# Performance work log

Measured on AMD Instinct MI355X. Metric: run time of the kernel, lower is better.

## Reference

```python
import jax, jax.numpy as jnp
import numpy as np

N = 50000        # nodes
E = 1_600_000    # edges per graph (avg degree 32)
T = 5            # timesteps per node
F_RAW = 395      # 3 meta channels + 392 signal
H_GRU = 64
HID = 40


def setup_inputs() -> dict:
    key = jax.random.key(0)
    ks = jax.random.split(key, 20)
    s = 0.05
    inp = {
        "x": jax.random.normal(ks[0], (N, T, F_RAW), jnp.float32),
        "edge_index": jax.random.randint(ks[1], (2, E), 0, N, dtype=jnp.int32),
        "feat_edge_index": jax.random.randint(ks[2], (2, E), 0, N, dtype=jnp.int32),
        # FeatureCNN: Conv1d(1, 16, kernel_size=40, stride=88) -> L=5 -> flatten 80
        "conv_w": jax.random.normal(ks[3], (16, 1, 40), jnp.float32) * s,
        "conv_b": jnp.zeros((16,), jnp.float32),
        "lin1_w": jax.random.normal(ks[4], (40, 80), jnp.float32) * s,
        "lin1_b": jnp.zeros((40,), jnp.float32),
        # GRU(input=41, hidden=64), PyTorch gate order: r, z, n
        "gru_w_ih": jax.random.normal(ks[5], (3 * H_GRU, 41), jnp.float32) * s,
        "gru_w_hh": jax.random.normal(ks[6], (3 * H_GRU, H_GRU), jnp.float32) * s,
        "gru_b_ih": jnp.zeros((3 * H_GRU,), jnp.float32),
        "gru_b_hh": jnp.zeros((3 * H_GRU,), jnp.float32),
        "gcn1_w": jax.random.normal(ks[7], (104, HID), jnp.float32) * s,
        "gcn1_b": jnp.zeros((HID,), jnp.float32),
        "gcn2_w": jax.random.normal(ks[8], (104, HID), jnp.float32) * s,
        "gcn2_b": jnp.zeros((HID,), jnp.float32),
        "mlp_w": jax.random.normal(ks[9], (1, 2 * HID), jnp.float32) * s,
        "mlp_b": jnp.zeros((1,), jnp.float32),
    }
    return inp


def _gcn(h_in, ei, W, b):
    """GCNConv: sym-normalized sum aggregation with self-loops."""
    n = h_in.shape[0]
    h = h_in @ W                                   # [n, out]
    loops = jnp.arange(n, dtype=ei.dtype)
    src = jnp.concatenate([ei[0], loops])
    dst = jnp.concatenate([ei[1], loops])
    deg = jax.ops.segment_sum(jnp.ones_like(dst, h.dtype), dst, num_segments=n)
    dinv = jax.lax.rsqrt(jnp.maximum(deg, 1.0))    # deg >= 1 due to self-loops
    norm = dinv[src] * dinv[dst]                   # [E+n]
    msg = h[src] * norm[:, None]                   # gather + scale
    return jax.ops.segment_sum(msg, dst, num_segments=n) + b


def _cnn_gru(x, conv_w, conv_b, lin1_w, lin1_b, gru_w_ih, gru_w_hh, gru_b_ih, gru_b_hh):
    n = x.shape[0]
    y = x[:, :, 2].reshape(-1, 1)                  # [n*5, 1]
    sig = x[:, :, 3:].reshape(-1, 1, 392)          # [n*5, 1, 392]
    # FeatureCNN: conv1d k=40 s=88 -> [n*5, 16, 5] -> relu -> flatten 80
    c = jax.lax.conv_general_dilated(
        sig, conv_w, window_strides=(88,), padding="VALID",
        dimension_numbers=("NCH", "OIH", "NCH"))
    c = jax.nn.relu(c + conv_b[None, :, None]).reshape(-1, 80)
    out = jax.nn.relu(c @ lin1_w.T + lin1_b)       # [n*5, 40]
    seq = jnp.concatenate([out, y], axis=1).reshape(n, 5, 41)

    def gru_step(h, xt):
        gi = xt @ gru_w_ih.T + gru_b_ih            # [n, 192]
        gh = h @ gru_w_hh.T + gru_b_hh
        ir, iz, inn = jnp.split(gi, 3, axis=1)
        hr, hz, hn_ = jnp.split(gh, 3, axis=1)
        r = jax.nn.sigmoid(ir + hr)
        z = jax.nn.sigmoid(iz + hz)
        ng = jnp.tanh(inn + r * hn_)
        h = (1.0 - z) * ng + z * h
        return h, None

    h0 = jnp.zeros((n, H_GRU), x.dtype)
    hn, _ = jax.lax.scan(gru_step, h0, jnp.swapaxes(seq[:, :4, :], 0, 1))
    return jnp.concatenate([seq[:, 4, :-1], hn], axis=1)  # [n, 104]


def reference(x, edge_index, feat_edge_index, conv_w, conv_b, lin1_w, lin1_b,
              gru_w_ih, gru_w_hh, gru_b_ih, gru_b_hh,
              gcn1_w, gcn1_b, gcn2_w, gcn2_b, mlp_w, mlp_b):
    feats = _cnn_gru(x, conv_w, conv_b, lin1_w, lin1_b,
                     gru_w_ih, gru_w_hh, gru_b_ih, gru_b_hh)   # [N, 104]
    emb1 = jax.nn.relu(_gcn(feats, edge_index, gcn1_w, gcn1_b))      # [N, 40]
    emb2 = jax.nn.relu(_gcn(feats, feat_edge_index, gcn2_w, gcn2_b)) # [N, 40]
    emb = jnp.concatenate([emb1, emb2], axis=1)                      # [N, 80]
    return emb @ mlp_w.T + mlp_b                                     # [N, 1]
```

## Files before the change

### kernel.cpp

```cpp
#include <hip/hip_runtime.h>
#include <hip/hip_fp16.h>
#include <math.h>


#define NB      512
#define MAXNPB  104
#define PART_T  4096

__global__ __launch_bounds__(512) void k_cnn(
    const float* __restrict__ x,
    const float* __restrict__ conv_w,
    const float* __restrict__ conv_b,
    const float* __restrict__ lin_w,
    const float* __restrict__ lin_b,
    float* __restrict__ seq,
    float* __restrict__ feats,
    int nrows, int nnodes)
{
    __shared__ __align__(16) float smem[64 * 200];
    __shared__ __align__(16) float s_cw[16][44];
    __shared__ __align__(16) float s_lw[40][84];
    __shared__ float s_cb[16];
    __shared__ float s_lb[40];

    const int tid = threadIdx.x;
    const int r0  = blockIdx.x * 64;

    float sg[25];
    #pragma unroll
    for (int it = 0; it < 25; ++it) {
        int i = tid + it * 512;
        int row = i / 200, e = i - row * 200;
        int p = e / 40, kk = e - p * 40;
        int gr = r0 + row; if (gr >= nrows) gr = nrows - 1;
        sg[it] = x[(size_t)gr * 395 + 3 + 88 * p + kk];
    }

    for (int i = tid; i < 640;  i += 512) s_cw[i / 40][i % 40] = conv_w[i];
    for (int i = tid; i < 3200; i += 512) s_lw[i / 80][i % 80] = lin_w[i];
    if (tid < 16) s_cb[tid] = conv_b[tid];
    if (tid >= 64 && tid < 104) s_lb[tid - 64] = lin_b[tid - 64];

    if (tid < 64) {
        int gr = r0 + tid;
        if (gr < nrows) {
            float y = x[(size_t)gr * 395 + 2];
            int node = gr / 5, t = gr - node * 5;
            if (t < 4) seq[(t * nnodes + node) * 41 + 40] = y;
        }
    }

    #pragma unroll
    for (int it = 0; it < 25; ++it) {
        int i = tid + it * 512;
        int row = i / 200, e = i - row * 200;
        smem[row * 200 + e] = sg[it];
    }
    __syncthreads();

    const int row = tid >> 3, cg = tid & 7;
    float creg[2][5];
    {
        float acc[2][5];
        #pragma unroll
        for (int cc = 0; cc < 2; ++cc) {
            float b = s_cb[2 * cg + cc];
            #pragma unroll
            for (int p = 0; p < 5; ++p) acc[cc][p] = b;
        }
        #pragma unroll
        for (int k4 = 0; k4 < 40; k4 += 4) {
            float4 sv[5];
            #pragma unroll
            for (int p = 0; p < 5; ++p)
                sv[p] = *(const float4*)&smem[row * 200 + p * 40 + k4];
            #pragma unroll
            for (int cc = 0; cc < 2; ++cc) {
                float4 w4 = *(const float4*)&s_cw[2 * cg + cc][k4];
                #pragma unroll
                for (int p = 0; p < 5; ++p)
                    acc[cc][p] += w4.x * sv[p].x + w4.y * sv[p].y + w4.z * sv[p].z + w4.w * sv[p].w;
            }
        }
        #pragma unroll
        for (int cc = 0; cc < 2; ++cc)
            #pragma unroll
            for (int p = 0; p < 5; ++p) creg[cc][p] = fmaxf(acc[cc][p], 0.0f);
    }
    __syncthreads();

    #pragma unroll
    for (int cc = 0; cc < 2; ++cc)
        #pragma unroll
        for (int p = 0; p < 5; ++p)
            smem[row * 84 + (2 * cg + cc) * 5 + p] = creg[cc][p];
    __syncthreads();

    {
        const int jg = tid & 7;
        float acc[5];
        #pragma unroll
        for (int jj = 0; jj < 5; ++jj) acc[jj] = s_lb[5 * jg + jj];
        #pragma unroll
        for (int i4 = 0; i4 < 80; i4 += 4) {
            float4 c0 = *(const float4*)&smem[row * 84 + i4];
            #pragma unroll
            for (int jj = 0; jj < 5; ++jj) {
                float4 w4 = *(const float4*)&s_lw[5 * jg + jj][i4];
                acc[jj] += w4.x * c0.x + w4.y * c0.y + w4.z * c0.z + w4.w * c0.w;
            }
        }
        int gr = r0 + row;
        if (gr < nrows) {
            int node = gr / 5, t = gr - node * 5;
            #pragma unroll
            for (int jj = 0; jj < 5; ++jj) {
                float v = fmaxf(acc[jj], 0.0f);
                if (t < 4) seq[(t * nnodes + node) * 41 + 5 * jg + jj] = v;
                else       feats[node * 104 + 5 * jg + jj] = v;
            }
        }
    }
}

__global__ __launch_bounds__(512) void k_gru(
    const float* __restrict__ seq,
    const float* __restrict__ w_ih,
    const float* __restrict__ w_hh,
    const float* __restrict__ b_ih,
    const float* __restrict__ b_hh,
    float* __restrict__ feats,
    int nnodes)
{
    __shared__ __align__(16) float s_wi[41][192];
    __shared__ __align__(16) float s_wh[64][192];
    __shared__ __align__(16) float s_h[64][132];
    __shared__ __align__(16) float s_x[41][132];
    __shared__ float s_bi[192], s_bh[192];

    const int tid  = threadIdx.x;
    const int nblk = blockIdx.x * 128;

    float xr[11];
    #pragma unroll
    for (int r = 0; r < 11; ++r) {
        int i = tid + r * 512;
        if (i < 5248) {
            int nl = i / 41, k = i - nl * 41;
            int node = nblk + nl; if (node >= nnodes) node = nnodes - 1;
            xr[r] = seq[(size_t)(0 * nnodes + node) * 41 + k];
        }
    }

    for (int i = tid; i < 192 * 41; i += 512) { int g = i / 41, k = i - g * 41; s_wi[k][g] = w_ih[i]; }
    for (int i = tid; i < 192 * 64; i += 512) { int g = i >> 6,  k = i & 63;    s_wh[k][g] = w_hh[i]; }
    if (tid < 192) { s_bi[tid] = b_ih[tid]; s_bh[tid] = b_hh[tid]; }
    for (int i = tid; i < 64 * 132; i += 512) ((float*)s_h)[i] = 0.0f;

    #pragma unroll
    for (int r = 0; r < 11; ++r) {
        int i = tid + r * 512;
        if (i < 5248) { int nl = i / 41, k = i - nl * 41; s_x[k][nl] = xr[r]; }
    }
    __syncthreads();

    const int jg = tid & 31, ngp = tid >> 5;
    const int j0 = 2 * jg, n0 = 8 * ngp;

    float hreg[2][8];
    #pragma unroll
    for (int a = 0; a < 2; ++a)
        #pragma unroll
        for (int b = 0; b < 8; ++b) hreg[a][b] = 0.0f;

    for (int t = 0; t < 4; ++t) {
        if (t < 3) {
            #pragma unroll
            for (int r = 0; r < 11; ++r) {
                int i = tid + r * 512;
                if (i < 5248) {
                    int nl = i / 41, k = i - nl * 41;
                    int node = nblk + nl; if (node >= nnodes) node = nnodes - 1;
                    xr[r] = seq[(size_t)((t + 1) * nnodes + node) * 41 + k];
                }
            }
        }

        float ar[2][8], az[2][8], ani[2][8], anh[2][8];
        #pragma unroll
        for (int a = 0; a < 2; ++a)
            #pragma unroll
            for (int b = 0; b < 8; ++b) { ar[a][b]=0.f; az[a][b]=0.f; ani[a][b]=0.f; anh[a][b]=0.f; }

        for (int k = 0; k < 41; ++k) {
            float4 xa = *(const float4*)&s_x[k][n0];
            float4 xb = *(const float4*)&s_x[k][n0 + 4];
            float xv[8] = {xa.x,xa.y,xa.z,xa.w,xb.x,xb.y,xb.z,xb.w};
            float2 wr = *(const float2*)&s_wi[k][j0];
            float2 wz = *(const float2*)&s_wi[k][64 + j0];
            float2 wn = *(const float2*)&s_wi[k][128 + j0];
            #pragma unroll
            for (int nn = 0; nn < 8; ++nn) {
                ar[0][nn] += wr.x*xv[nn]; ar[1][nn] += wr.y*xv[nn];
                az[0][nn] += wz.x*xv[nn]; az[1][nn] += wz.y*xv[nn];
                ani[0][nn]+= wn.x*xv[nn]; ani[1][nn]+= wn.y*xv[nn];
            }
        }
        for (int k = 0; k < 64; ++k) {
            float4 ha = *(const float4*)&s_h[k][n0];
            float4 hb = *(const float4*)&s_h[k][n0 + 4];
            float hv[8] = {ha.x,ha.y,ha.z,ha.w,hb.x,hb.y,hb.z,hb.w};
            float2 wr = *(const float2*)&s_wh[k][j0];
            float2 wz = *(const float2*)&s_wh[k][64 + j0];
            float2 wn = *(const float2*)&s_wh[k][128 + j0];
            #pragma unroll
            for (int nn = 0; nn < 8; ++nn) {
                ar[0][nn] += wr.x*hv[nn]; ar[1][nn] += wr.y*hv[nn];
                az[0][nn] += wz.x*hv[nn]; az[1][nn] += wz.y*hv[nn];
                anh[0][nn]+= wn.x*hv[nn]; anh[1][nn]+= wn.y*hv[nn];
            }
        }

        #pragma unroll
        for (int jj = 0; jj < 2; ++jj) {
            int j = j0 + jj;
            float br  = s_bi[j]      + s_bh[j];
            float bz  = s_bi[64 + j] + s_bh[64 + j];
            float bin = s_bi[128 + j], bhn = s_bh[128 + j];
            #pragma unroll
            for (int nn = 0; nn < 8; ++nn) {
                float r = 1.0f / (1.0f + expf(-(ar[jj][nn] + br)));
                float z = 1.0f / (1.0f + expf(-(az[jj][nn] + bz)));
                float g = tanhf(ani[jj][nn] + bin + r * (anh[jj][nn] + bhn));
                hreg[jj][nn] = (1.0f - z) * g + z * hreg[jj][nn];
            }
        }
        __syncthreads();

        if (t < 3) {
            #pragma unroll
            for (int jj = 0; jj < 2; ++jj) {
                *(float4*)&s_h[j0+jj][n0]     = make_float4(hreg[jj][0],hreg[jj][1],hreg[jj][2],hreg[jj][3]);
                *(float4*)&s_h[j0+jj][n0 + 4] = make_float4(hreg[jj][4],hreg[jj][5],hreg[jj][6],hreg[jj][7]);
            }
            #pragma unroll
            for (int r = 0; r < 11; ++r) {
                int i = tid + r * 512;
                if (i < 5248) { int nl = i / 41, k = i - nl * 41; s_x[k][nl] = xr[r]; }
            }
            __syncthreads();
        }
    }

    #pragma unroll
    for (int jj = 0; jj < 2; ++jj)
        #pragma unroll
        for (int nn = 0; nn < 8; ++nn) {
            int node = nblk + n0 + nn;
            if (node < nnodes) feats[node * 104 + 40 + j0 + jj] = hreg[jj][nn];
        }
}

__global__ __launch_bounds__(256) void k_hw(
    const float* __restrict__ feats,
    const float* __restrict__ w1,
    const float* __restrict__ w2,
    const float* __restrict__ dinv1,
    const float* __restrict__ dinv2,
    __half* __restrict__ hs1,
    __half* __restrict__ hs2,
    int nnodes)
{
    __shared__ __align__(16) float s_f[128][108];
    __shared__ __align__(16) float s_w[80][108];
    __shared__ float s_d[2][128];

    const int tid  = threadIdx.x;
    const int nblk = blockIdx.x * 128;

    for (int i = tid; i < 128 * 104; i += 256) {
        int n = i / 104, k = i - n * 104;
        int node = nblk + n; if (node >= nnodes) node = nnodes - 1;
        s_f[n][k] = feats[node * 104 + k];
    }
    for (int i = tid; i < 80 * 104; i += 256) {
        int o = i / 104, k = i - o * 104;
        s_w[o][k] = (o < 40) ? w1[k * 40 + o] : w2[k * 40 + (o - 40)];
    }
    if (tid < 128) {
        int node = nblk + tid; if (node >= nnodes) node = nnodes - 1;
        s_d[0][tid] = dinv1[node]; s_d[1][tid] = dinv2[node];
    }
    __syncthreads();

    const int og = tid & 7, ngp = tid >> 3;
    const int o0 = 10 * og, n0 = 4 * ngp;
    float acc[4][10];
    #pragma unroll
    for (int a = 0; a < 4; ++a)
        #pragma unroll
        for (int b = 0; b < 10; ++b) acc[a][b] = 0.0f;

    for (int k4 = 0; k4 < 104; k4 += 4) {
        float4 f[4];
        #pragma unroll
        for (int nn = 0; nn < 4; ++nn) f[nn] = *(const float4*)&s_f[n0 + nn][k4];
        #pragma unroll
        for (int oo = 0; oo < 10; ++oo) {
            float4 w4 = *(const float4*)&s_w[o0 + oo][k4];
            #pragma unroll
            for (int nn = 0; nn < 4; ++nn)
                acc[nn][oo] += w4.x * f[nn].x + w4.y * f[nn].y + w4.z * f[nn].z + w4.w * f[nn].w;
        }
    }
    #pragma unroll
    for (int nn = 0; nn < 4; ++nn) {
        int node = nblk + n0 + nn;
        if (node >= nnodes) continue;
        #pragma unroll
        for (int oo = 0; oo < 10; oo += 2) {
            int o = o0 + oo;
            float dscale = (o < 40) ? s_d[0][n0 + nn] : s_d[1][n0 + nn];
            __half2 h2 = __floats2half2_rn(dscale * acc[nn][oo], dscale * acc[nn][oo + 1]);
            if (o < 40) *(__half2*)&hs1[node * 40 + o]        = h2;
            else        *(__half2*)&hs2[node * 40 + (o - 40)] = h2;
        }
    }
}

__global__ void k_zero2(int* a, int* b, int n) {
    int i = blockIdx.x * 256 + threadIdx.x;
    if (i < n) { a[i] = 0; b[i] = 0; }
}

__global__ void k_deg(const int* __restrict__ d1, const int* __restrict__ d2,
                      int* c1, int* c2, int E) {
    int i = blockIdx.x * 256 + threadIdx.x;
    if (i < E) { atomicAdd(&c1[d1[i]], 1); atomicAdd(&c2[d2[i]], 1); }
}

__global__ __launch_bounds__(1024) void k_scan2(
    const int* __restrict__ cnt1, int* __restrict__ roff1, float* __restrict__ dinv1,
    const int* __restrict__ cnt2, int* __restrict__ roff2, float* __restrict__ dinv2,
    int n)
{
    const int* cnt  = blockIdx.x ? cnt2  : cnt1;
    int*       roff = blockIdx.x ? roff2 : roff1;
    float*     dinv = blockIdx.x ? dinv2 : dinv1;

    __shared__ int sp[1024];
    int t = threadIdx.x;
    int C = (n + 1023) >> 10;
    int i0 = t * C, i1 = min(i0 + C, n);
    int s = 0;
    for (int i = i0; i < i1; ++i) s += cnt[i];
    sp[t] = s;
    __syncthreads();
    for (int off = 1; off < 1024; off <<= 1) {
        int v = (t >= off) ? sp[t - off] : 0;
        __syncthreads();
        sp[t] += v;
        __syncthreads();
    }
    int run = sp[t] - s;
    for (int i = i0; i < i1; ++i) {
        int c = cnt[i];
        roff[i] = run;
        dinv[i] = rsqrtf((float)(c + 1));
        run += c;
    }
    if (t == 1023) roff[n] = sp[1023];
}

__global__ __launch_bounds__(512) void k_bcur(
    const int* __restrict__ roff1, const int* __restrict__ roff2,
    int* __restrict__ bcur, int npb, int n) {
    int b = threadIdx.x;
    if (b < NB) {
        int lo = min(b * npb, n);
        bcur[b]      = roff1[lo];
        bcur[NB + b] = roff2[lo];
    }
}

__global__ __launch_bounds__(256) void k_part(
    const int* __restrict__ e,
    int* __restrict__ bcur,
    unsigned long long* __restrict__ pairs,
    int E, int npb)
{
    __shared__ unsigned long long s_ed[PART_T];
    __shared__ int s_cnt[NB], s_base[NB], s_cur[NB];
    const int tid = threadIdx.x;
    const int e0  = blockIdx.x * PART_T;
    const int ne  = min(PART_T, E - e0);

    for (int i = tid; i < NB; i += 256) { s_cnt[i] = 0; s_cur[i] = 0; }
    __syncthreads();

    for (int k = tid; k < ne; k += 256) {
        int s = e[e0 + k], d = e[E + e0 + k];
        s_ed[k] = ((unsigned long long)(unsigned)d << 32) | (unsigned)s;
        atomicAdd(&s_cnt[d / npb], 1);
    }
    __syncthreads();
    for (int b = tid; b < NB; b += 256)
        if (s_cnt[b] > 0) s_base[b] = atomicAdd(&bcur[b], s_cnt[b]);
    __syncthreads();
    for (int k = tid; k < ne; k += 256) {
        unsigned long long p = s_ed[k];
        int b = (int)(p >> 32) / npb;
        int r = atomicAdd(&s_cur[b], 1);
        pairs[s_base[b] + r] = p;
    }
}

__global__ __launch_bounds__(256) void k_scatter3(
    const unsigned long long* __restrict__ pairs,
    const int* __restrict__ roff, int* __restrict__ csr,
    int n, int npb)
{
    __shared__ int s_cur[MAXNPB];
    const int tid = threadIdx.x;
    const int b   = blockIdx.x;
    const int lo  = b * npb;
    if (lo >= n) return;
    const int hi = min(lo + npb, n);
    const int nd = hi - lo;

    for (int i = tid; i < nd; i += 256) s_cur[i] = roff[lo + i];
    __syncthreads();

    const int seg0 = roff[lo], seg1 = roff[hi];
    for (int p = seg0 + tid; p < seg1; p += 256) {
        unsigned long long pr = pairs[p];
        int d = (int)(pr >> 32), s = (int)(pr & 0xffffffffu);
        int pos = atomicAdd(&s_cur[d - lo], 1);
        csr[pos] = s;
    }
}

__global__ __launch_bounds__(512) void k_agg(
    const __half* __restrict__ hs, const int* __restrict__ csr,
    const int* __restrict__ roff, const float* __restrict__ dinv,
    const float* __restrict__ bias, const float* __restrict__ mw,
    const float* __restrict__ mlp_b, float* __restrict__ out,
    int n, int accumulate)
{
    int wv = threadIdx.x >> 6, lane = threadIdx.x & 63;
    int d = blockIdx.x * 8 + wv;
    if (d >= n) return;
    int beg = roff[d], end = roff[d + 1];
    int fc = lane < 40 ? lane : 0;
    float acc = 0.0f;
    int e = beg;
    for (; e + 8 <= end; e += 8) {
        int s0 = csr[e],     s1 = csr[e + 1], s2 = csr[e + 2], s3 = csr[e + 3];
        int s4 = csr[e + 4], s5 = csr[e + 5], s6 = csr[e + 6], s7 = csr[e + 7];
        float a0 = __half2float(hs[(size_t)s0 * 40 + fc]);
        float a1 = __half2float(hs[(size_t)s1 * 40 + fc]);
        float a2 = __half2float(hs[(size_t)s2 * 40 + fc]);
        float a3 = __half2float(hs[(size_t)s3 * 40 + fc]);
        float a4 = __half2float(hs[(size_t)s4 * 40 + fc]);
        float a5 = __half2float(hs[(size_t)s5 * 40 + fc]);
        float a6 = __half2float(hs[(size_t)s6 * 40 + fc]);
        float a7 = __half2float(hs[(size_t)s7 * 40 + fc]);
        acc += ((a0 + a1) + (a2 + a3)) + ((a4 + a5) + (a6 + a7));
    }
    for (; e < end; ++e) acc += __half2float(hs[(size_t)csr[e] * 40 + fc]);

    float v = dinv[d] * (__half2float(hs[(size_t)d * 40 + fc]) + acc) + bias[fc];
    v = fmaxf(v, 0.0f) * mw[fc];
    if (lane >= 40) v = 0.0f;
    #pragma unroll
    for (int off = 32; off > 0; off >>= 1) v += __shfl_down(v, off);
    if (lane == 0)
        out[d] = accumulate ? (out[d] + v) : (mlp_b[0] + v);
}

extern "C" void kernel_launch(void* const* d_in, const int* in_sizes, int n_in,
                              void* d_out, int out_size, void* d_ws, size_t ws_size,
                              hipStream_t stream)
{
    const float* x      = (const float*)d_in[0];
    const int*   ei1    = (const int*)d_in[1];
    const int*   ei2    = (const int*)d_in[2];
    const float* conv_w = (const float*)d_in[3];
    const float* conv_b = (const float*)d_in[4];
    const float* lin_w  = (const float*)d_in[5];
    const float* lin_b  = (const float*)d_in[6];
    const float* w_ih   = (const float*)d_in[7];
    const float* w_hh   = (const float*)d_in[8];
    const float* b_ih   = (const float*)d_in[9];
    const float* b_hh   = (const float*)d_in[10];
    const float* g1w    = (const float*)d_in[11];
    const float* g1b    = (const float*)d_in[12];
    const float* g2w    = (const float*)d_in[13];
    const float* g2b    = (const float*)d_in[14];
    const float* mw     = (const float*)d_in[15];
    const float* mb     = (const float*)d_in[16];

    const int N = in_sizes[0] / (5 * 395);
    const int E = in_sizes[1] / 2;
    const int R = N * 5;
    float* out = (float*)d_out;

    const int npb = (N + NB - 1) / NB;
    if (npb > MAXNPB) return;

    char* wp = (char*)d_ws;
    auto alloc = [&](size_t bytes) {
        char* p = wp; wp += (bytes + 255) & ~(size_t)255; return p;
    };
    size_t seq_bytes = (size_t)4 * N * 41 * 4;
    float*  seq   = (float*)alloc(seq_bytes);
    float*  feats = (float*)alloc((size_t)N * 104 * 4);
    __half* hs1   = (__half*)alloc((size_t)N * 40 * 2);
    __half* hs2   = (__half*)alloc((size_t)N * 40 * 2);
    int*    csr1  = (int*)alloc((size_t)E * 4);
    int*    csr2  = (int*)alloc((size_t)E * 4);
    int*    cnt1  = (int*)alloc((size_t)N * 4);
    int*    cnt2  = (int*)alloc((size_t)N * 4);
    int*    roff1 = (int*)alloc((size_t)(N + 1) * 4);
    int*    roff2 = (int*)alloc((size_t)(N + 1) * 4);
    float*  dinv1 = (float*)alloc((size_t)N * 4);
    float*  dinv2 = (float*)alloc((size_t)N * 4);
    int*    bcur  = (int*)alloc((size_t)2 * NB * 4);

    unsigned long long *pairs1, *pairs2;
    if (2 * (size_t)E * 8 <= seq_bytes) {
        pairs1 = (unsigned long long*)seq;
        pairs2 = pairs1 + E;
    } else {
        pairs1 = (unsigned long long*)alloc((size_t)E * 8);
        pairs2 = (unsigned long long*)alloc((size_t)E * 8);
    }
    if ((size_t)(wp - (char*)d_ws) > ws_size) return;

    hipLaunchKernelGGL(k_zero2,    dim3((N + 255) / 256), dim3(256), 0, stream, cnt1, cnt2, N);
    hipLaunchKernelGGL(k_deg,      dim3((E + 255) / 256), dim3(256), 0, stream, ei1 + E, ei2 + E, cnt1, cnt2, E);
    hipLaunchKernelGGL(k_scan2,    dim3(2), dim3(1024), 0, stream, cnt1, roff1, dinv1, cnt2, roff2, dinv2, N);
    hipLaunchKernelGGL(k_bcur,     dim3(1), dim3(NB), 0, stream, roff1, roff2, bcur, npb, N);
    hipLaunchKernelGGL(k_part,     dim3((E + PART_T - 1) / PART_T), dim3(256), 0, stream, ei1, bcur,      pairs1, E, npb);
    hipLaunchKernelGGL(k_part,     dim3((E + PART_T - 1) / PART_T), dim3(256), 0, stream, ei2, bcur + NB, pairs2, E, npb);
    hipLaunchKernelGGL(k_scatter3, dim3(NB), dim3(256), 0, stream, pairs1, roff1, csr1, N, npb);
    hipLaunchKernelGGL(k_scatter3, dim3(NB), dim3(256), 0, stream, pairs2, roff2, csr2, N, npb);
    hipLaunchKernelGGL(k_cnn,      dim3((R + 63) / 64), dim3(512), 0, stream, x, conv_w, conv_b, lin_w, lin_b, seq, feats, R, N);
    hipLaunchKernelGGL(k_gru,      dim3((N + 127) / 128), dim3(512), 0, stream, seq, w_ih, w_hh, b_ih, b_hh, feats, N);
    hipLaunchKernelGGL(k_hw,       dim3((N + 127) / 128), dim3(256), 0, stream, feats, g1w, g2w, dinv1, dinv2, hs1, hs2, N);
    hipLaunchKernelGGL(k_agg,      dim3((N + 7) / 8), dim3(512), 0, stream, hs1, csr1, roff1, dinv1, g1b, mw,      mb, out, N, 0);
    hipLaunchKernelGGL(k_agg,      dim3((N + 7) / 8), dim3(512), 0, stream, hs2, csr2, roff2, dinv2, g2b, mw + 40, mb, out, N, 1);
}
```

Measured before the change: 748.1 us.

## Shrink GRU tile to 96 nodes with fp16 shared weights; fold bcur into scan

The GRU kernel now processes 96 nodes per block instead of 128 and stores input weights, recurrent weights and x in shared memory as fp16. Converting back to fp32 on load cuts LDS footprint and per-thread registers, which should allow more resident blocks and spread the work over more blocks. The separate bucket-cursor kernel is merged into the scan kernel, saving one launch. The cost is reduced precision for weights and inputs, extra conversion instructions, and narrower float2 shared loads in place of float4.

Measured after the change: 824.9 us. +10.3%, slower.

```diff
diff --git a/kernel.cpp b/kernel.cpp
--- a/kernel.cpp
+++ b/kernel.cpp
@@ -6,6 +6,7 @@
 #define NB      512
 #define MAXNPB  104
 #define PART_T  4096
+#define GN      96
 
 __global__ __launch_bounds__(512) void k_cnn(
     const float* __restrict__ x,
@@ -132,53 +133,53 @@
     float* __restrict__ feats,
     int nnodes)
 {
-    __shared__ __align__(16) float s_wi[41][192];
-    __shared__ __align__(16) float s_wh[64][192];
-    __shared__ __align__(16) float s_h[64][132];
-    __shared__ __align__(16) float s_x[41][132];
+    __shared__ __align__(16) __half s_wi[41][192];
+    __shared__ __align__(16) __half s_wh[64][192];
+    __shared__ __align__(16) float  s_h[64][104];
+    __shared__ __align__(16) __half s_x[41][104];
     __shared__ float s_bi[192], s_bh[192];
 
     const int tid  = threadIdx.x;
-    const int nblk = blockIdx.x * 128;
-
-    float xr[11];
-    #pragma unroll
-    for (int r = 0; r < 11; ++r) {
+    const int nblk = blockIdx.x * GN;
+
+    float xr[8];
+    #pragma unroll
+    for (int r = 0; r < 8; ++r) {
         int i = tid + r * 512;
-        if (i < 5248) {
+        if (i < GN * 41) {
             int nl = i / 41, k = i - nl * 41;
             int node = nblk + nl; if (node >= nnodes) node = nnodes - 1;
-            xr[r] = seq[(size_t)(0 * nnodes + node) * 41 + k];
-        }
-    }
-
-    for (int i = tid; i < 192 * 41; i += 512) { int g = i / 41, k = i - g * 41; s_wi[k][g] = w_ih[i]; }
-    for (int i = tid; i < 192 * 64; i += 512) { int g = i >> 6,  k = i & 63;    s_wh[k][g] = w_hh[i]; }
+            xr[r] = seq[(size_t)node * 41 + k];
+        }
+    }
+
+    for (int i = tid; i < 192 * 41; i += 512) { int g = i / 41, k = i - g * 41; s_wi[k][g] = __float2half(w_ih[i]); }
+    for (int i = tid; i < 192 * 64; i += 512) { int g = i >> 6,  k = i & 63;    s_wh[k][g] = __float2half(w_hh[i]); }
     if (tid < 192) { s_bi[tid] = b_ih[tid]; s_bh[tid] = b_hh[tid]; }
-    for (int i = tid; i < 64 * 132; i += 512) ((float*)s_h)[i] = 0.0f;
-
-    #pragma unroll
-    for (int r = 0; r < 11; ++r) {
+    for (int i = tid; i < 64 * 104; i += 512) ((float*)s_h)[i] = 0.0f;
+
+    #pragma unroll
+    for (int r = 0; r < 8; ++r) {
         int i = tid + r * 512;
-        if (i < 5248) { int nl = i / 41, k = i - nl * 41; s_x[k][nl] = xr[r]; }
+        if (i < GN * 41) { int nl = i / 41, k = i - nl * 41; s_x[k][nl] = __float2half(xr[r]); }
     }
     __syncthreads();
 
     const int jg = tid & 31, ngp = tid >> 5;
-    const int j0 = 2 * jg, n0 = 8 * ngp;
-
-    float hreg[2][8];
+    const int j0 = 2 * jg, n0 = 6 * ngp;
+
+    float hreg[2][6];
     #pragma unroll
     for (int a = 0; a < 2; ++a)
         #pragma unroll
-        for (int b = 0; b < 8; ++b) hreg[a][b] = 0.0f;
+        for (int b = 0; b < 6; ++b) hreg[a][b] = 0.0f;
 
     for (int t = 0; t < 4; ++t) {
         if (t < 3) {
             #pragma unroll
-            for (int r = 0; r < 11; ++r) {
+            for (int r = 0; r < 8; ++r) {
                 int i = tid + r * 512;
-                if (i < 5248) {
+                if (i < GN * 41) {
                     int nl = i / 41, k = i - nl * 41;
                     int node = nblk + nl; if (node >= nnodes) node = nnodes - 1;
                     xr[r] = seq[(size_t)((t + 1) * nnodes + node) * 41 + k];
@@ -186,35 +187,37 @@
             }
         }
 
-        float ar[2][8], az[2][8], ani[2][8], anh[2][8];
+        float ar[2][6], az[2][6], ani[2][6], anh[2][6];
         #pragma unroll
         for (int a = 0; a < 2; ++a)
             #pragma unroll
-            for (int b = 0; b < 8; ++b) { ar[a][b]=0.f; az[a][b]=0.f; ani[a][b]=0.f; anh[a][b]=0.f; }
+            for (int b = 0; b < 6; ++b) { ar[a][b]=0.f; az[a][b]=0.f; ani[a][b]=0.f; anh[a][b]=0.f; }
 
         for (int k = 0; k < 41; ++k) {
-            float4 xa = *(const float4*)&s_x[k][n0];
-            float4 xb = *(const float4*)&s_x[k][n0 + 4];
-            float xv[8] = {xa.x,xa.y,xa.z,xa.w,xb.x,xb.y,xb.z,xb.w};
-            float2 wr = *(const float2*)&s_wi[k][j0];
-            float2 wz = *(const float2*)&s_wi[k][64 + j0];
-            float2 wn = *(const float2*)&s_wi[k][128 + j0];
-            #pragma unroll
-            for (int nn = 0; nn < 8; ++nn) {
+            float2 x01 = __half22float2(*(const __half2*)&s_x[k][n0]);
+            float2 x23 = __half22float2(*(const __half2*)&s_x[k][n0 + 2]);
+            float2 x45 = __half22float2(*(const __half2*)&s_x[k][n0 + 4]);
+            float xv[6] = {x01.x, x01.y, x23.x, x23.y, x45.x, x45.y};
+            float2 wr = __half22float2(*(const __half2*)&s_wi[k][j0]);
+            float2 wz = __half22float2(*(const __half2*)&s_wi[k][64 + j0]);
+            float2 wn = __half22float2(*(const __half2*)&s_wi[k][128 + j0]);
+            #pragma unroll
+            for (int nn = 0; nn < 6; ++nn) {
                 ar[0][nn] += wr.x*xv[nn]; ar[1][nn] += wr.y*xv[nn];
                 az[0][nn] += wz.x*xv[nn]; az[1][nn] += wz.y*xv[nn];
                 ani[0][nn]+= wn.x*xv[nn]; ani[1][nn]+= wn.y*xv[nn];
             }
         }
         for (int k = 0; k < 64; ++k) {
-            float4 ha = *(const float4*)&s_h[k][n0];
-            float4 hb = *(const float4*)&s_h[k][n0 + 4];
-            float hv[8] = {ha.x,ha.y,ha.z,ha.w,hb.x,hb.y,hb.z,hb.w};
-            float2 wr = *(const float2*)&s_wh[k][j0];
-            float2 wz = *(const float2*)&s_wh[k][64 + j0];
-            float2 wn = *(const float2*)&s_wh[k][128 + j0];
-            #pragma unroll
-            for (int nn = 0; nn < 8; ++nn) {
+            float2 h01 = *(const float2*)&s_h[k][n0];
+            float2 h23 = *(const float2*)&s_h[k][n0 + 2];
+            float2 h45 = *(const float2*)&s_h[k][n0 + 4];
+            float hv[6] = {h01.x, h01.y, h23.x, h23.y, h45.x, h45.y};
+            float2 wr = __half22float2(*(const __half2*)&s_wh[k][j0]);
+            float2 wz = __half22float2(*(const __half2*)&s_wh[k][64 + j0]);
+            float2 wn = __half22float2(*(const __half2*)&s_wh[k][128 + j0]);
+            #pragma unroll
+            for (int nn = 0; nn < 6; ++nn) {
                 ar[0][nn] += wr.x*hv[nn]; ar[1][nn] += wr.y*hv[nn];
                 az[0][nn] += wz.x*hv[nn]; az[1][nn] += wz.y*hv[nn];
                 anh[0][nn]+= wn.x*hv[nn]; anh[1][nn]+= wn.y*hv[nn];
@@ -228,7 +231,7 @@
             float bz  = s_bi[64 + j] + s_bh[64 + j];
             float bin = s_bi[128 + j], bhn = s_bh[128 + j];
             #pragma unroll
-            for (int nn = 0; nn < 8; ++nn) {
+            for (int nn = 0; nn < 6; ++nn) {
                 float r = 1.0f / (1.0f + expf(-(ar[jj][nn] + br)));
                 float z = 1.0f / (1.0f + expf(-(az[jj][nn] + bz)));
                 float g = tanhf(ani[jj][nn] + bin + r * (anh[jj][nn] + bhn));
@@ -240,13 +243,14 @@
         if (t < 3) {
             #pragma unroll
             for (int jj = 0; jj < 2; ++jj) {
-                *(float4*)&s_h[j0+jj][n0]     = make_float4(hreg[jj][0],hreg[jj][1],hreg[jj][2],hreg[jj][3]);
-                *(float4*)&s_h[j0+jj][n0 + 4] = make_float4(hreg[jj][4],hreg[jj][5],hreg[jj][6],hreg[jj][7]);
-            }
-            #pragma unroll
-            for (int r = 0; r < 11; ++r) {
+                *(float2*)&s_h[j0 + jj][n0]     = make_float2(hreg[jj][0], hreg[jj][1]);
+                *(float2*)&s_h[j0 + jj][n0 + 2] = make_float2(hreg[jj][2], hreg[jj][3]);
+                *(float2*)&s_h[j0 + jj][n0 + 4] = make_float2(hreg[jj][4], hreg[jj][5]);
+            }
+            #pragma unroll
+            for (int r = 0; r < 8; ++r) {
                 int i = tid + r * 512;
-                if (i < 5248) { int nl = i / 41, k = i - nl * 41; s_x[k][nl] = xr[r]; }
+                if (i < GN * 41) { int nl = i / 41, k = i - nl * 41; s_x[k][nl] = __float2half(xr[r]); }
             }
             __syncthreads();
         }
@@ -255,7 +259,7 @@
     #pragma unroll
     for (int jj = 0; jj < 2; ++jj)
         #pragma unroll
-        for (int nn = 0; nn < 8; ++nn) {
+        for (int nn = 0; nn < 6; ++nn) {
             int node = nblk + n0 + nn;
             if (node < nnodes) feats[node * 104 + 40 + j0 + jj] = hreg[jj][nn];
         }
@@ -342,11 +346,12 @@
 __global__ __launch_bounds__(1024) void k_scan2(
     const int* __restrict__ cnt1, int* __restrict__ roff1, float* __restrict__ dinv1,
     const int* __restrict__ cnt2, int* __restrict__ roff2, float* __restrict__ dinv2,
-    int n)
+    int* __restrict__ bcur, int npb, int n)
 {
     const int* cnt  = blockIdx.x ? cnt2  : cnt1;
     int*       roff = blockIdx.x ? roff2 : roff1;
     float*     dinv = blockIdx.x ? dinv2 : dinv1;
+    int*       bc   = bcur + (blockIdx.x ? NB : 0);
 
     __shared__ int sp[1024];
     int t = threadIdx.x;
@@ -370,16 +375,10 @@
         run += c;
     }
     if (t == 1023) roff[n] = sp[1023];
-}
-
-__global__ __launch_bounds__(512) void k_bcur(
-    const int* __restrict__ roff1, const int* __restrict__ roff2,
-    int* __restrict__ bcur, int npb, int n) {
-    int b = threadIdx.x;
-    if (b < NB) {
-        int lo = min(b * npb, n);
-        bcur[b]      = roff1[lo];
-        bcur[NB + b] = roff2[lo];
+    __syncthreads();
+    if (t < NB) {
+        int lo = min(t * npb, n);
+        bc[t] = roff[lo];
     }
 }
 
@@ -539,14 +538,13 @@
 
     hipLaunchKernelGGL(k_zero2,    dim3((N + 255) / 256), dim3(256), 0, stream, cnt1, cnt2, N);
     hipLaunchKernelGGL(k_deg,      dim3((E + 255) / 256), dim3(256), 0, stream, ei1 + E, ei2 + E, cnt1, cnt2, E);
-    hipLaunchKernelGGL(k_scan2,    dim3(2), dim3(1024), 0, stream, cnt1, roff1, dinv1, cnt2, roff2, dinv2, N);
-    hipLaunchKernelGGL(k_bcur,     dim3(1), dim3(NB), 0, stream, roff1, roff2, bcur, npb, N);
+    hipLaunchKernelGGL(k_scan2,    dim3(2), dim3(1024), 0, stream, cnt1, roff1, dinv1, cnt2, roff2, dinv2, bcur, npb, N);
     hipLaunchKernelGGL(k_part,     dim3((E + PART_T - 1) / PART_T), dim3(256), 0, stream, ei1, bcur,      pairs1, E, npb);
     hipLaunchKernelGGL(k_part,     dim3((E + PART_T - 1) / PART_T), dim3(256), 0, stream, ei2, bcur + NB, pairs2, E, npb);
     hipLaunchKernelGGL(k_scatter3, dim3(NB), dim3(256), 0, stream, pairs1, roff1, csr1, N, npb);
     hipLaunchKernelGGL(k_scatter3, dim3(NB), dim3(256), 0, stream, pairs2, roff2, csr2, N, npb);
     hipLaunchKernelGGL(k_cnn,      dim3((R + 63) / 64), dim3(512), 0, stream, x, conv_w, conv_b, lin_w, lin_b, seq, feats, R, N);
-    hipLaunchKernelGGL(k_gru,      dim3((N + 127) / 128), dim3(512), 0, stream, seq, w_ih, w_hh, b_ih, b_hh, feats, N);
+    hipLaunchKernelGGL(k_gru,      dim3((N + GN - 1) / GN), dim3(512), 0, stream, seq, w_ih, w_hh, b_ih, b_hh, feats, N);
     hipLaunchKernelGGL(k_hw,       dim3((N + 127) / 128), dim3(256), 0, stream, feats, g1w, g2w, dinv1, dinv2, hs1, hs2, N);
     hipLaunchKernelGGL(k_agg,      dim3((N + 7) / 8), dim3(512), 0, stream, hs1, csr1, roff1, dinv1, g1b, mw,      mb, out, N, 0);
     hipLaunchKernelGGL(k_agg,      dim3((N + 7) / 8), dim3(512), 0, stream, hs2, csr2, roff2, dinv2, g2b, mw + 40, mb, out, N, 1);
```
